# Optimization experiments

Hardware: AMD Instinct MI355X
Metric: run time of the kernel (lower is better)

The kernel has to match this reference:

```python
import math
import jax, jax.numpy as jnp
import numpy as np

SQ = 2048   # sequence length (hard-coded in source views)
B = 1       # batch (input_[:, 0, :] in QKVLinear)
H = 2048    # HIDDEN_SIZE
NH = 16     # NUM_HEADS
HD = 128    # head dim


def setup_inputs() -> dict:
    key = jax.random.key(0)
    ks = jax.random.split(key, 8)
    hidden_states = jax.random.normal(ks[0], (SQ, B, H), dtype=jnp.float32)
    # causal mask: True = masked (upper triangle, strictly above diagonal)
    attention_mask = jnp.triu(jnp.ones((SQ, SQ), dtype=bool), k=1)[None, None]
    qkv_w = jax.random.normal(ks[1], (3 * H, H), dtype=jnp.float32) * 0.02
    qkv_b = jax.random.normal(ks[2], (3 * H,), dtype=jnp.float32) * 0.02
    # SVD rotation matrices (approximately norm-preserving random matrices)
    svd_token = jax.random.normal(ks[3], (H, H), dtype=jnp.float32) / math.sqrt(H)
    svd_qk = jax.random.normal(ks[4], (NH, HD, HD), dtype=jnp.float32) / math.sqrt(HD)
    svd_vlin = jax.random.normal(ks[5], (NH, HD, HD), dtype=jnp.float32) / math.sqrt(HD)
    dense_w = jax.random.normal(ks[6], (NH, HD, H), dtype=jnp.float32) * 0.02
    dense_b = jax.random.normal(ks[7], (H,), dtype=jnp.float32) * 0.02
    return {
        "hidden_states": hidden_states,
        "attention_mask": attention_mask,
        "qkv_w": qkv_w,
        "qkv_b": qkv_b,
        "svd_token": svd_token,
        "svd_qk": svd_qk,
        "svd_vlin": svd_vlin,
        "dense_w": dense_w,
        "dense_b": dense_b,
    }


def reference(hidden_states, attention_mask, qkv_w, qkv_b, svd_token,
              svd_qk, svd_vlin, dense_w, dense_b):
    # QKVLinear: project input and weight through token-SVD (drop fraction = 0 -> no zeroing)
    x = hidden_states[:, 0, :] @ svd_token                 # [sq, H]
    w = qkv_w @ svd_token                                  # [3H, H]
    mixed = x @ w.T + qkv_b                                # [sq, 3H]
    mixed = mixed.reshape(SQ, B, NH, 3 * HD)
    q, k, v = jnp.split(mixed, 3, axis=-1)                 # each [sq, b, nh, hd]

    # per-head SVD-rotated Q/K (qk_drop = 0 -> h_mask is all-False, no zeroing)
    q = jnp.einsum('sbhd,hde->sbhe', q, svd_qk)
    k = jnp.einsum('sbhd,hde->sbhe', k, svd_qk)

    # scores: baddbmm with alpha = 1/(sqrt(hd)*coeff), then softmax rescales by coeff;
    # with layer_num=1 coeff=1, masked positions end at exactly -10000.
    scale = 1.0 / math.sqrt(HD)
    scores = jnp.einsum('sbhd,tbhd->bhst', q, k) * scale   # [b, nh, sq, sq]
    scores = jnp.where(attention_mask, -10000.0, scores)
    probs = jax.nn.softmax(scores, axis=-1)                # dropout in eval mode (identity)

    # per-head SVD-rotated V (vlinear_drop = 0 -> no zeroing)
    vv = jnp.einsum('sbhd,hde->sbhe', v, svd_vlin)
    ctx = jnp.einsum('bhst,tbhe->sbhe', probs, vv).reshape(SQ, B, H)

    # AttnOutputLinear: tsr block for head h = (dense_w[h].T @ svd_vlin[h]).T = svd_vlin[h].T @ dense_w[h]
    tsr = jnp.einsum('hde,hdo->heo', svd_vlin, dense_w).reshape(H, H)
    out = ctx @ tsr + dense_b                              # [sq, b, H]
    return out
```

## Files before the change

### kernel.cpp

```cpp
#include <hip/hip_runtime.h>
#include <hip/hip_bf16.h>
#include <stdint.h>
#include <math.h>


typedef __bf16 bf16_t;
typedef __bf16 bf16x8 __attribute__((ext_vector_type(8)));
typedef __bf16 bf16x4 __attribute__((ext_vector_type(4)));
typedef float  f32x4  __attribute__((ext_vector_type(4)));

__device__ __forceinline__ void async16(const void* g, void* l) {
  __builtin_amdgcn_global_load_lds(
      (const __attribute__((address_space(1))) void*)(uintptr_t)g,
      (__attribute__((address_space(3))) void*)(uint32_t)(uintptr_t)l,
      16, 0, 0);
}

__global__ __launch_bounds__(256)
void gemm_nt128(const bf16_t* __restrict__ A, const bf16_t* __restrict__ B,
                void* __restrict__ Cv, const void* __restrict__ biasv,
                int K, int lda, int ldb, int ldc, float alpha, int flags)
{
  const int bm0 = blockIdx.y * 128;
  const int bn0 = blockIdx.x * 128;

  __shared__ bf16_t shA[8192];
  __shared__ bf16_t shB[8192];

  const int t  = threadIdx.x;
  const int w  = t >> 6;
  const int l  = t & 63;
  const int wm = (w >> 1) * 64;
  const int wn = (w & 1) * 64;
  const int r0 = l >> 2;
  const int c0 = ((l & 3) ^ ((l >> 3) & 3)) * 8;
  const int fr = l & 15;
  const int kc = l >> 4;
  const int swr = ((fr >> 1) & 3);

  f32x4 acc[4][4];
  #pragma unroll
  for (int i = 0; i < 4; ++i)
    #pragma unroll
    for (int j = 0; j < 4; ++j)
      #pragma unroll
      for (int r = 0; r < 4; ++r)
        acc[i][j][r] = 0.0f;

  for (int k0 = 0; k0 < K; k0 += 64) {
    #pragma unroll
    for (int u = 0; u < 4; ++u) {
      const int seg  = u * 4 + w;
      const int half = seg >> 3;
      const int s8   = seg & 7;
      const int row  = s8 * 16 + r0;
      const int gk   = k0 + half * 32 + c0;
      async16(A + (long long)(bm0 + row) * lda + gk, &shA[half * 4096 + s8 * 512]);
      async16(B + (long long)(bn0 + row) * ldb + gk, &shB[half * 4096 + s8 * 512]);
    }
    __builtin_amdgcn_s_waitcnt(0);
    __syncthreads();

    const int rc = (kc ^ swr) * 8;
    #pragma unroll
    for (int h = 0; h < 2; ++h) {
      bf16x8 af[4], bfv[4];
      #pragma unroll
      for (int i = 0; i < 4; ++i) {
        af[i]  = *(const bf16x8*)&shA[h * 4096 + (wm + i * 16 + fr) * 32 + rc];
        bfv[i] = *(const bf16x8*)&shB[h * 4096 + (wn + i * 16 + fr) * 32 + rc];
      }
      #pragma unroll
      for (int i = 0; i < 4; ++i)
        #pragma unroll
        for (int j = 0; j < 4; ++j)
          acc[i][j] = __builtin_amdgcn_mfma_f32_16x16x32_bf16(af[i], bfv[j], acc[i][j], 0, 0, 0);
    }
    __syncthreads();
  }

  const int cc = l & 15;
  const int rq = (l >> 4) * 4;
  if (flags & 4) {
    float* C = (float*)Cv;
    const float* bias = (const float*)biasv;
    #pragma unroll
    for (int j = 0; j < 4; ++j) {
      const int col = bn0 + wn + j * 16 + cc;
      const float bv = bias ? bias[col] : 0.0f;
      #pragma unroll
      for (int i = 0; i < 4; ++i)
        #pragma unroll
        for (int r = 0; r < 4; ++r) {
          const int row = bm0 + wm + i * 16 + rq + r;
          C[(long long)row * ldc + col] = acc[i][j][r] * alpha + bv;
        }
    }
  } else {
    bf16_t* C = (bf16_t*)Cv;
    const bf16_t* bias = (flags & 8) ? (const bf16_t*)biasv : nullptr;
    #pragma unroll
    for (int j = 0; j < 4; ++j) {
      const int col = bn0 + wn + j * 16 + cc;
      const float bv = bias ? (float)bias[col] : 0.0f;
      #pragma unroll
      for (int i = 0; i < 4; ++i)
        #pragma unroll
        for (int r = 0; r < 4; ++r) {
          const int row = bm0 + wm + i * 16 + rq + r;
          C[(long long)row * ldc + col] = (bf16_t)(acc[i][j][r] * alpha + bv);
        }
    }
  }
}

__global__ __launch_bounds__(256)
void gemm_nt64(const bf16_t* __restrict__ A, const bf16_t* __restrict__ B,
               void* __restrict__ Cv, const void* __restrict__ biasv,
               int K, int lda, int ldb, int ldc, float alpha, int flags)
{
  const int bm0 = blockIdx.y * 64;
  const int bn0 = blockIdx.x * 128;

  __shared__ bf16_t shA[4096];
  __shared__ bf16_t shB[8192];

  const int t  = threadIdx.x;
  const int w  = t >> 6;
  const int l  = t & 63;
  const int wm = (w >> 1) * 32;
  const int wn = (w & 1) * 64;
  const int r0 = l >> 2;
  const int c0 = ((l & 3) ^ ((l >> 3) & 3)) * 8;
  const int fr = l & 15;
  const int kc = l >> 4;
  const int swr = ((fr >> 1) & 3);

  f32x4 acc[2][4];
  #pragma unroll
  for (int i = 0; i < 2; ++i)
    #pragma unroll
    for (int j = 0; j < 4; ++j)
      #pragma unroll
      for (int r = 0; r < 4; ++r)
        acc[i][j][r] = 0.0f;

  for (int k0 = 0; k0 < K; k0 += 64) {
    #pragma unroll
    for (int u = 0; u < 2; ++u) {
      const int seg  = u * 4 + w;
      const int half = seg >> 2;
      const int s4   = seg & 3;
      const int row  = s4 * 16 + r0;
      async16(A + (long long)(bm0 + row) * lda + (k0 + half * 32 + c0),
              &shA[half * 2048 + s4 * 512]);
    }
    #pragma unroll
    for (int u = 0; u < 4; ++u) {
      const int seg  = u * 4 + w;
      const int half = seg >> 3;
      const int s8   = seg & 7;
      const int row  = s8 * 16 + r0;
      async16(B + (long long)(bn0 + row) * ldb + (k0 + half * 32 + c0),
              &shB[half * 4096 + s8 * 512]);
    }
    __builtin_amdgcn_s_waitcnt(0);
    __syncthreads();

    const int rc = (kc ^ swr) * 8;
    #pragma unroll
    for (int h = 0; h < 2; ++h) {
      bf16x8 af[2], bfv[4];
      #pragma unroll
      for (int i = 0; i < 2; ++i)
        af[i]  = *(const bf16x8*)&shA[h * 2048 + (wm + i * 16 + fr) * 32 + rc];
      #pragma unroll
      for (int j = 0; j < 4; ++j)
        bfv[j] = *(const bf16x8*)&shB[h * 4096 + (wn + j * 16 + fr) * 32 + rc];
      #pragma unroll
      for (int i = 0; i < 2; ++i)
        #pragma unroll
        for (int j = 0; j < 4; ++j)
          acc[i][j] = __builtin_amdgcn_mfma_f32_16x16x32_bf16(af[i], bfv[j], acc[i][j], 0, 0, 0);
    }
    __syncthreads();
  }

  const int cc = l & 15;
  const int rq = (l >> 4) * 4;
  if (flags & 4) {
    float* C = (float*)Cv;
    const float* bias = (const float*)biasv;
    #pragma unroll
    for (int j = 0; j < 4; ++j) {
      const int col = bn0 + wn + j * 16 + cc;
      const float bv = bias ? bias[col] : 0.0f;
      #pragma unroll
      for (int i = 0; i < 2; ++i)
        #pragma unroll
        for (int r = 0; r < 4; ++r) {
          const int row = bm0 + wm + i * 16 + rq + r;
          C[(long long)row * ldc + col] = acc[i][j][r] * alpha + bv;
        }
    }
  } else {
    bf16_t* C = (bf16_t*)Cv;
    #pragma unroll
    for (int j = 0; j < 4; ++j) {
      const int col = bn0 + wn + j * 16 + cc;
      #pragma unroll
      for (int i = 0; i < 2; ++i)
        #pragma unroll
        for (int r = 0; r < 4; ++r) {
          const int row = bm0 + wm + i * 16 + rq + r;
          C[(long long)row * ldc + col] = (bf16_t)(acc[i][j][r] * alpha);
        }
    }
  }
}

__global__ __launch_bounds__(256)
void gemm_prep(const bf16_t* __restrict__ qkT, const bf16_t* __restrict__ vlT,
               const bf16_t* __restrict__ qkv_wT, const bf16_t* __restrict__ dwT,
               bf16_t* __restrict__ Wrot, bf16_t* __restrict__ tsrT)
{
  const int z = blockIdx.z;
  const bf16_t* A;
  const bf16_t* B;
  bf16_t* C;
  int bm0, bn0;
  if (z < 48) {
    const int h = z / 3, p = z - 3 * h;
    A = (p == 2 ? vlT : qkT) + h * 16384;
    B = qkv_wT + (long long)z * 262144;
    C = Wrot + (long long)z * 262144;
    bm0 = 0;
    bn0 = blockIdx.x * 128;
  } else {
    const int b = z - 48;
    A = dwT + (long long)b * 262144;
    B = vlT + b * 16384;
    C = tsrT;
    bm0 = blockIdx.x * 128;
    bn0 = b * 128;
  }

  __shared__ bf16_t shA[8192];
  __shared__ bf16_t shB[8192];

  const int t  = threadIdx.x;
  const int w  = t >> 6;
  const int l  = t & 63;
  const int wm = (w >> 1) * 64;
  const int wn = (w & 1) * 64;
  const int r0 = l >> 2;
  const int c0 = ((l & 3) ^ ((l >> 3) & 3)) * 8;
  const int fr = l & 15;
  const int kc = l >> 4;
  const int swr = ((fr >> 1) & 3);
  const int arow0 = (z < 48 ? 0 : bm0);
  const int brow0 = (z < 48 ? bn0 : 0);

  f32x4 acc[4][4];
  #pragma unroll
  for (int i = 0; i < 4; ++i)
    #pragma unroll
    for (int j = 0; j < 4; ++j)
      #pragma unroll
      for (int r = 0; r < 4; ++r)
        acc[i][j][r] = 0.0f;

  for (int k0 = 0; k0 < 128; k0 += 64) {
    #pragma unroll
    for (int u = 0; u < 4; ++u) {
      const int seg  = u * 4 + w;
      const int half = seg >> 3;
      const int s8   = seg & 7;
      const int row  = s8 * 16 + r0;
      const int gk   = k0 + half * 32 + c0;
      async16(A + (long long)(arow0 + row) * 128 + gk, &shA[half * 4096 + s8 * 512]);
      async16(B + (long long)(brow0 + row) * 128 + gk, &shB[half * 4096 + s8 * 512]);
    }
    __builtin_amdgcn_s_waitcnt(0);
    __syncthreads();

    const int rc = (kc ^ swr) * 8;
    #pragma unroll
    for (int h = 0; h < 2; ++h) {
      bf16x8 af[4], bfv[4];
      #pragma unroll
      for (int i = 0; i < 4; ++i) {
        af[i]  = *(const bf16x8*)&shA[h * 4096 + (wm + i * 16 + fr) * 32 + rc];
        bfv[i] = *(const bf16x8*)&shB[h * 4096 + (wn + i * 16 + fr) * 32 + rc];
      }
      #pragma unroll
      for (int i = 0; i < 4; ++i)
        #pragma unroll
        for (int j = 0; j < 4; ++j)
          acc[i][j] = __builtin_amdgcn_mfma_f32_16x16x32_bf16(af[i], bfv[j], acc[i][j], 0, 0, 0);
    }
    __syncthreads();
  }

  const int cc = l & 15;
  const int rq = (l >> 4) * 4;
  #pragma unroll
  for (int j = 0; j < 4; ++j) {
    const int col = bn0 + wn + j * 16 + cc;
    #pragma unroll
    for (int i = 0; i < 4; ++i)
      #pragma unroll
      for (int r = 0; r < 4; ++r) {
        const int row = arow0 + wm + i * 16 + rq + r;
        C[(long long)row * 2048 + col] = (bf16_t)acc[i][j][r];
      }
  }
}

__global__ __launch_bounds__(256)
void flash_k(const bf16_t* __restrict__ mixed, const bf16_t* __restrict__ vT,
             bf16_t* __restrict__ ctx, float iscale)
{
  const int h  = blockIdx.y;
  const int qt = 31 - (int)blockIdx.x;
  const int r0g = qt * 64;
  const int niter = (qt >> 1) + 1;
  const bf16_t* Qp = mixed + h * 384;
  const bf16_t* Kp = mixed + h * 384 + 128;
  const bf16_t* Vp = vT + (long long)h * 262144;

  __shared__ bf16_t sKV[128 * 128];
  __shared__ bf16_t sP[64 * 136];
  __shared__ float  sL[2][64];

  const int t  = threadIdx.x;
  const int w  = t >> 6;
  const int l  = t & 63;
  const int wm = (w >> 1) * 32;
  const int wn = (w & 1) * 64;
  const int fr = l & 15;
  const int kc = l >> 4;

  bf16x8 aq[2][4];
  #pragma unroll
  for (int i = 0; i < 2; ++i)
    #pragma unroll
    for (int ks = 0; ks < 4; ++ks)
      aq[i][ks] = *(const bf16x8*)(Qp + (long long)(r0g + wm + i * 16 + fr) * 6144
                                      + ks * 32 + kc * 8);

  f32x4 oacc[2][4];
  #pragma unroll
  for (int i = 0; i < 2; ++i)
    #pragma unroll
    for (int j = 0; j < 4; ++j)
      #pragma unroll
      for (int r = 0; r < 4; ++r) oacc[i][j][r] = 0.0f;
  float lsum[2][4];
  #pragma unroll
  for (int i = 0; i < 2; ++i)
    #pragma unroll
    for (int r = 0; r < 4; ++r) lsum[i][r] = 0.0f;

  for (int it = 0; it < niter; ++it) {
    const int t0 = it * 128;
    #pragma unroll
    for (int s = 0; s < 8; ++s) {
      const int chunk = (w * 8 + s) * 64 + l;
      const int r = chunk >> 4;
      const int c = (chunk & 15) ^ (r & 7);
      async16(Kp + (long long)(t0 + r) * 6144 + c * 8, &sKV[(w * 8 + s) * 512]);
    }
    __builtin_amdgcn_s_waitcnt(0);
    __syncthreads();

    f32x4 acc[2][4];
    #pragma unroll
    for (int i = 0; i < 2; ++i)
      #pragma unroll
      for (int j = 0; j < 4; ++j)
        #pragma unroll
        for (int r = 0; r < 4; ++r) acc[i][j][r] = 0.0f;
    #pragma unroll
    for (int ks = 0; ks < 4; ++ks) {
      bf16x8 bk[4];
      #pragma unroll
      for (int j = 0; j < 4; ++j) {
        const int r = wn + j * 16 + fr;
        const int c = (ks * 4 + kc) ^ (r & 7);
        bk[j] = *(const bf16x8*)&sKV[r * 128 + c * 8];
      }
      #pragma unroll
      for (int i = 0; i < 2; ++i)
        #pragma unroll
        for (int j = 0; j < 4; ++j)
          acc[i][j] = __builtin_amdgcn_mfma_f32_16x16x32_bf16(aq[i][ks], bk[j], acc[i][j], 0, 0, 0);
    }

    #pragma unroll
    for (int i = 0; i < 2; ++i) {
      #pragma unroll
      for (int r = 0; r < 4; ++r) {
        const int rowl = wm + i * 16 + kc * 4 + r;
        const int Rg = r0g + rowl;
        float rs = 0.f;
        #pragma unroll
        for (int j = 0; j < 4; ++j) {
          const int coll = wn + j * 16 + fr;
          const float e = (t0 + coll <= Rg) ? __expf(acc[i][j][r] * iscale) : 0.0f;
          rs += e;
          sP[rowl * 136 + coll] = (bf16_t)e;
        }
        rs += __shfl_xor(rs, 1, 64);
        rs += __shfl_xor(rs, 2, 64);
        rs += __shfl_xor(rs, 4, 64);
        rs += __shfl_xor(rs, 8, 64);
        if (fr == 0) sL[w & 1][rowl] = rs;
      }
    }
    __syncthreads();

    #pragma unroll
    for (int i = 0; i < 2; ++i)
      #pragma unroll
      for (int r = 0; r < 4; ++r) {
        const int rowl = wm + i * 16 + kc * 4 + r;
        lsum[i][r] += sL[0][rowl] + sL[1][rowl];
      }
    #pragma unroll
    for (int s = 0; s < 8; ++s) {
      const int chunk = (w * 8 + s) * 64 + l;
      const int r = chunk >> 4;
      const int c = (chunk & 15) ^ (r & 7);
      async16(Vp + (long long)r * 2048 + t0 + c * 8, &sKV[(w * 8 + s) * 512]);
    }
    __builtin_amdgcn_s_waitcnt(0);
    __syncthreads();

    #pragma unroll
    for (int ks = 0; ks < 4; ++ks) {
      bf16x8 ap[2], bv[4];
      #pragma unroll
      for (int i = 0; i < 2; ++i)
        ap[i] = *(const bf16x8*)&sP[(wm + i * 16 + fr) * 136 + ks * 32 + kc * 8];
      #pragma unroll
      for (int j = 0; j < 4; ++j) {
        const int r = wn + j * 16 + fr;
        const int c = (ks * 4 + kc) ^ (r & 7);
        bv[j] = *(const bf16x8*)&sKV[r * 128 + c * 8];
      }
      #pragma unroll
      for (int i = 0; i < 2; ++i)
        #pragma unroll
        for (int j = 0; j < 4; ++j)
          oacc[i][j] = __builtin_amdgcn_mfma_f32_16x16x32_bf16(ap[i], bv[j], oacc[i][j], 0, 0, 0);
    }
    __syncthreads();
  }

  #pragma unroll
  for (int i = 0; i < 2; ++i) {
    #pragma unroll
    for (int r = 0; r < 4; ++r) {
      const int rowl = wm + i * 16 + kc * 4 + r;
      const float inv = 1.0f / lsum[i][r];
      #pragma unroll
      for (int j = 0; j < 4; ++j) {
        const int coll = wn + j * 16 + fr;
        ctx[(long long)(r0g + rowl) * 2048 + h * 128 + coll] = (bf16_t)(oacc[i][j][r] * inv);
      }
    }
  }
}

__global__ __launch_bounds__(256)
void cvt2_f2b(const float* __restrict__ a, bf16_t* __restrict__ oa,
              const float* __restrict__ b, bf16_t* __restrict__ ob, int n)
{
  const float* in = blockIdx.y ? b : a;
  bf16_t* out = blockIdx.y ? ob : oa;
  const int i = (blockIdx.x * 256 + threadIdx.x) * 4;
  if (i >= n) return;
  const f32x4 v = *(const f32x4*)(in + i);
  bf16x4 o;
  #pragma unroll
  for (int j = 0; j < 4; ++j) o[j] = (bf16_t)v[j];
  *(bf16x4*)(out + i) = o;
}

__global__ __launch_bounds__(256)
void transpose_k2(const float* __restrict__ in1, const float* __restrict__ in2,
                  bf16_t* __restrict__ o1, bf16_t* __restrict__ o2)
{
  __shared__ bf16_t sm[32][33];
  const int z  = blockIdx.z;
  const float* ip = (z < 48) ? in1 + (long long)z * 262144
                             : in2 + (long long)(z - 48) * 262144;
  bf16_t* op = (z < 48) ? o1 + (long long)z * 262144
                        : o2 + (long long)(z - 48) * 262144;
  const int r0 = blockIdx.x << 5;
  const int c0 = blockIdx.y << 5;
  const int tx = threadIdx.x & 31;
  const int ty = threadIdx.x >> 5;
  #pragma unroll
  for (int yy = ty; yy < 32; yy += 8)
    sm[yy][tx] = (bf16_t)ip[(long long)(r0 + yy) * 2048 + c0 + tx];
  __syncthreads();
  #pragma unroll
  for (int yy = ty; yy < 32; yy += 8)
    op[(long long)(c0 + yy) * 128 + r0 + tx] = sm[tx][yy];
}

__global__ __launch_bounds__(256)
void transpose_rot(const float* __restrict__ qk, const float* __restrict__ vl,
                   bf16_t* __restrict__ oqk, bf16_t* __restrict__ ovl)
{
  __shared__ bf16_t sm[32][33];
  const int z  = blockIdx.z;
  const float* ip = (z < 16 ? qk : vl) + (long long)(z & 15) * 16384;
  bf16_t* op = (z < 16 ? oqk : ovl) + (long long)(z & 15) * 16384;
  const int r0 = blockIdx.x << 5;
  const int c0 = blockIdx.y << 5;
  const int tx = threadIdx.x & 31;
  const int ty = threadIdx.x >> 5;
  #pragma unroll
  for (int yy = ty; yy < 32; yy += 8)
    sm[yy][tx] = (bf16_t)ip[(long long)(r0 + yy) * 128 + c0 + tx];
  __syncthreads();
  #pragma unroll
  for (int yy = ty; yy < 32; yy += 8)
    op[(long long)(c0 + yy) * 128 + r0 + tx] = sm[tx][yy];
}

__global__ __launch_bounds__(256)
void transpose_b2b(const bf16_t* __restrict__ in, bf16_t* __restrict__ out,
                   int R, long long zsi, int rsi, long long zso)
{
  __shared__ bf16_t sm[32][33];
  const int z  = blockIdx.z;
  const int r0 = blockIdx.x << 5;
  const int c0 = blockIdx.y << 5;
  const int tx = threadIdx.x & 31;
  const int ty = threadIdx.x >> 5;
  const bf16_t* ip = in + (long long)z * zsi;
  bf16_t* op = out + (long long)z * zso;
  #pragma unroll
  for (int yy = ty; yy < 32; yy += 8)
    sm[yy][tx] = ip[(long long)(r0 + yy) * rsi + c0 + tx];
  __syncthreads();
  #pragma unroll
  for (int yy = ty; yy < 32; yy += 8)
    op[(long long)(c0 + yy) * R + r0 + tx] = sm[tx][yy];
}

__global__ void brot_k(const float* __restrict__ qkv_b,
                       const float* __restrict__ svd_qk,
                       const float* __restrict__ svd_vl,
                       bf16_t* __restrict__ brot)
{
  const int hp = blockIdx.x;
  const int h = hp / 3, p = hp % 3;
  const int e = threadIdx.x;
  const float* R = (p == 2 ? svd_vl : svd_qk) + h * 16384;
  const float* b = qkv_b + h * 384 + p * 128;
  float acc = 0.f;
  for (int d = 0; d < 128; ++d)
    acc += b[d] * R[d * 128 + e];
  brot[h * 384 + p * 128 + e] = (bf16_t)acc;
}

extern "C" void kernel_launch(void* const* d_in, const int* in_sizes, int n_in,
                              void* d_out, int out_size, void* d_ws, size_t ws_size,
                              hipStream_t stream)
{
  const float* hs      = (const float*)d_in[0];
  const float* qkv_w   = (const float*)d_in[2];
  const float* qkv_b   = (const float*)d_in[3];
  const float* svd_tok = (const float*)d_in[4];
  const float* svd_qk  = (const float*)d_in[5];
  const float* svd_vl  = (const float*)d_in[6];
  const float* dense_w = (const float*)d_in[7];
  const float* dense_b = (const float*)d_in[8];
  float* out = (float*)d_out;
  bf16_t* ws = (bf16_t*)d_ws;

  bf16_t* hsb    = ws;
  bf16_t* stb    = ws +  4194304LL;
  bf16_t* Mbuf   = ws +  8388608LL;
  bf16_t* x2     = ws + 12582912LL;
  bf16_t* qkv_wT = ws + 16777216LL;
  bf16_t* Wrot   = ws + 29360128LL;
  bf16_t* mixed  = ws + 41943040LL;
  bf16_t* vT     = ws + 54525952LL;
  bf16_t* ctx    = ws + 58720256LL;
  bf16_t* dwT    = ws + 62914560LL;
  bf16_t* tsrT   = ws + 67108864LL;
  bf16_t* qkT    = ws + 71303168LL;
  bf16_t* vlT    = ws + 71565312LL;
  bf16_t* brot   = ws + 71827456LL;
  if (ws_size < 71833600ULL * 2ULL) return;

  const float iscale = 0.08838834764831845f;

  cvt2_f2b<<<dim3(4096, 2), 256, 0, stream>>>(hs, hsb, svd_tok, stb, 4194304);
  transpose_rot<<<dim3(4, 4, 32), 256, 0, stream>>>(svd_qk, svd_vl, qkT, vlT);
  transpose_k2<<<dim3(4, 64, 64), 256, 0, stream>>>(qkv_w, dense_w, qkv_wT, dwT);
  brot_k<<<dim3(48), 128, 0, stream>>>(qkv_b, svd_qk, svd_vl, brot);

  gemm_nt64<<<dim3(16, 32), 256, 0, stream>>>(stb, stb, Mbuf, nullptr,
      2048, 2048, 2048, 2048, 1.0f, 0);
  gemm_nt64<<<dim3(16, 32), 256, 0, stream>>>(hsb, Mbuf, x2, nullptr,
      2048, 2048, 2048, 2048, 1.0f, 0);
  gemm_prep<<<dim3(16, 1, 64), 256, 0, stream>>>(qkT, vlT, qkv_wT, dwT, Wrot, tsrT);
  gemm_nt128<<<dim3(48, 16), 256, 0, stream>>>(x2, Wrot, mixed, brot,
      2048, 2048, 2048, 6144, 1.0f, 8);
  transpose_b2b<<<dim3(64, 4, 16), 256, 0, stream>>>(mixed + 256, vT, 2048, 384, 6144, 262144);
  flash_k<<<dim3(32, 16), 256, 0, stream>>>(mixed, vT, ctx, iscale);
  gemm_nt64<<<dim3(16, 32), 256, 0, stream>>>(ctx, tsrT, out, dense_b,
      2048, 2048, 2048, 2048, 1.0f, 4);
}
```

Before: 438.1 us.

## Merge prep kernels into fused launches and deepen GEMM K-tile

Folds the four preprocessing kernels (convert, two transposes, bias rotation) into one front kernel, and merges the weight-rotation GEMM with the svd_token Gram GEMM (stb·stbᵀ) into a single launch of 1536 blocks. The 64x128 GEMM now stages 128-wide K tiles per iteration instead of 64, halving its barrier count but doubling shared memory. The goal is fewer launches and better overlap of small independent work, at the cost of lower occupancy and a weight-transpose path that loops over 64 tiles per block with less parallelism.

```diff
diff --git a/kernel.cpp b/kernel.cpp
--- a/kernel.cpp
+++ b/kernel.cpp
@@ -81,49 +81,32 @@
 
   const int cc = l & 15;
   const int rq = (l >> 4) * 4;
-  if (flags & 4) {
-    float* C = (float*)Cv;
-    const float* bias = (const float*)biasv;
-    #pragma unroll
-    for (int j = 0; j < 4; ++j) {
-      const int col = bn0 + wn + j * 16 + cc;
-      const float bv = bias ? bias[col] : 0.0f;
-      #pragma unroll
-      for (int i = 0; i < 4; ++i)
-        #pragma unroll
-        for (int r = 0; r < 4; ++r) {
-          const int row = bm0 + wm + i * 16 + rq + r;
-          C[(long long)row * ldc + col] = acc[i][j][r] * alpha + bv;
-        }
-    }
-  } else {
-    bf16_t* C = (bf16_t*)Cv;
-    const bf16_t* bias = (flags & 8) ? (const bf16_t*)biasv : nullptr;
-    #pragma unroll
-    for (int j = 0; j < 4; ++j) {
-      const int col = bn0 + wn + j * 16 + cc;
-      const float bv = bias ? (float)bias[col] : 0.0f;
-      #pragma unroll
-      for (int i = 0; i < 4; ++i)
-        #pragma unroll
-        for (int r = 0; r < 4; ++r) {
-          const int row = bm0 + wm + i * 16 + rq + r;
-          C[(long long)row * ldc + col] = (bf16_t)(acc[i][j][r] * alpha + bv);
-        }
-    }
+  bf16_t* C = (bf16_t*)Cv;
+  const bf16_t* bias = (flags & 8) ? (const bf16_t*)biasv : nullptr;
+  #pragma unroll
+  for (int j = 0; j < 4; ++j) {
+    const int col = bn0 + wn + j * 16 + cc;
+    const float bv = bias ? (float)bias[col] : 0.0f;
+    #pragma unroll
+    for (int i = 0; i < 4; ++i)
+      #pragma unroll
+      for (int r = 0; r < 4; ++r) {
+        const int row = bm0 + wm + i * 16 + rq + r;
+        C[(long long)row * ldc + col] = (bf16_t)(acc[i][j][r] * alpha + bv);
+      }
   }
 }
 
 __global__ __launch_bounds__(256)
-void gemm_nt64(const bf16_t* __restrict__ A, const bf16_t* __restrict__ B,
-               void* __restrict__ Cv, const void* __restrict__ biasv,
-               int K, int lda, int ldb, int ldc, float alpha, int flags)
+void gemm_nt64k(const bf16_t* __restrict__ A, const bf16_t* __restrict__ B,
+                void* __restrict__ Cv, const void* __restrict__ biasv,
+                int K, int lda, int ldb, int ldc, float alpha, int flags)
 {
   const int bm0 = blockIdx.y * 64;
   const int bn0 = blockIdx.x * 128;
 
-  __shared__ bf16_t shA[4096];
-  __shared__ bf16_t shB[8192];
+  __shared__ bf16_t shA[8192];
+  __shared__ bf16_t shB[16384];
 
   const int t  = threadIdx.x;
   const int w  = t >> 6;
@@ -145,38 +128,36 @@
       for (int r = 0; r < 4; ++r)
         acc[i][j][r] = 0.0f;
 
-  for (int k0 = 0; k0 < K; k0 += 64) {
-    #pragma unroll
-    for (int u = 0; u < 2; ++u) {
-      const int seg  = u * 4 + w;
-      const int half = seg >> 2;
-      const int s4   = seg & 3;
-      const int row  = s4 * 16 + r0;
-      async16(A + (long long)(bm0 + row) * lda + (k0 + half * 32 + c0),
-              &shA[half * 2048 + s4 * 512]);
-    }
+  for (int k0 = 0; k0 < K; k0 += 128) {
     #pragma unroll
     for (int u = 0; u < 4; ++u) {
-      const int seg  = u * 4 + w;
-      const int half = seg >> 3;
-      const int s8   = seg & 7;
-      const int row  = s8 * 16 + r0;
-      async16(B + (long long)(bn0 + row) * ldb + (k0 + half * 32 + c0),
-              &shB[half * 4096 + s8 * 512]);
+      const int seg = u * 4 + w;
+      const int q   = seg >> 2;
+      const int s4  = seg & 3;
+      async16(A + (long long)(bm0 + s4 * 16 + r0) * lda + (k0 + q * 32 + c0),
+              &shA[q * 2048 + s4 * 512]);
+    }
+    #pragma unroll
+    for (int u = 0; u < 8; ++u) {
+      const int seg = u * 4 + w;
+      const int q   = seg >> 3;
+      const int s8  = seg & 7;
+      async16(B + (long long)(bn0 + s8 * 16 + r0) * ldb + (k0 + q * 32 + c0),
+              &shB[q * 4096 + s8 * 512]);
     }
     __builtin_amdgcn_s_waitcnt(0);
     __syncthreads();
 
     const int rc = (kc ^ swr) * 8;
     #pragma unroll
-    for (int h = 0; h < 2; ++h) {
+    for (int q = 0; q < 4; ++q) {
       bf16x8 af[2], bfv[4];
       #pragma unroll
       for (int i = 0; i < 2; ++i)
-        af[i]  = *(const bf16x8*)&shA[h * 2048 + (wm + i * 16 + fr) * 32 + rc];
+        af[i]  = *(const bf16x8*)&shA[q * 2048 + (wm + i * 16 + fr) * 32 + rc];
       #pragma unroll
       for (int j = 0; j < 4; ++j)
-        bfv[j] = *(const bf16x8*)&shB[h * 4096 + (wn + j * 16 + fr) * 32 + rc];
+        bfv[j] = *(const bf16x8*)&shB[q * 4096 + (wn + j * 16 + fr) * 32 + rc];
       #pragma unroll
       for (int i = 0; i < 2; ++i)
         #pragma unroll
@@ -220,100 +201,170 @@
 }
 
 __global__ __launch_bounds__(256)
-void gemm_prep(const bf16_t* __restrict__ qkT, const bf16_t* __restrict__ vlT,
-               const bf16_t* __restrict__ qkv_wT, const bf16_t* __restrict__ dwT,
-               bf16_t* __restrict__ Wrot, bf16_t* __restrict__ tsrT)
+void gemm_mprep(const bf16_t* __restrict__ qkT, const bf16_t* __restrict__ vlT,
+                const bf16_t* __restrict__ qkv_wT, const bf16_t* __restrict__ dwT,
+                bf16_t* __restrict__ Wrot, bf16_t* __restrict__ tsrT,
+                const bf16_t* __restrict__ stb, bf16_t* __restrict__ Mbuf)
 {
-  const int z = blockIdx.z;
-  const bf16_t* A;
-  const bf16_t* B;
-  bf16_t* C;
-  int bm0, bn0;
-  if (z < 48) {
-    const int h = z / 3, p = z - 3 * h;
-    A = (p == 2 ? vlT : qkT) + h * 16384;
-    B = qkv_wT + (long long)z * 262144;
-    C = Wrot + (long long)z * 262144;
-    bm0 = 0;
-    bn0 = blockIdx.x * 128;
-  } else {
-    const int b = z - 48;
-    A = dwT + (long long)b * 262144;
-    B = vlT + b * 16384;
-    C = tsrT;
-    bm0 = blockIdx.x * 128;
-    bn0 = b * 128;
-  }
-
-  __shared__ bf16_t shA[8192];
-  __shared__ bf16_t shB[8192];
-
+  __shared__ bf16_t smem[16384];
+  const int z = blockIdx.x;
   const int t  = threadIdx.x;
   const int w  = t >> 6;
   const int l  = t & 63;
-  const int wm = (w >> 1) * 64;
-  const int wn = (w & 1) * 64;
   const int r0 = l >> 2;
   const int c0 = ((l & 3) ^ ((l >> 3) & 3)) * 8;
   const int fr = l & 15;
   const int kc = l >> 4;
   const int swr = ((fr >> 1) & 3);
-  const int arow0 = (z < 48 ? 0 : bm0);
-  const int brow0 = (z < 48 ? bn0 : 0);
-
-  f32x4 acc[4][4];
-  #pragma unroll
-  for (int i = 0; i < 4; ++i)
-    #pragma unroll
-    for (int j = 0; j < 4; ++j)
-      #pragma unroll
-      for (int r = 0; r < 4; ++r)
-        acc[i][j][r] = 0.0f;
-
-  for (int k0 = 0; k0 < 128; k0 += 64) {
-    #pragma unroll
-    for (int u = 0; u < 4; ++u) {
-      const int seg  = u * 4 + w;
-      const int half = seg >> 3;
-      const int s8   = seg & 7;
-      const int row  = s8 * 16 + r0;
-      const int gk   = k0 + half * 32 + c0;
-      async16(A + (long long)(arow0 + row) * 128 + gk, &shA[half * 4096 + s8 * 512]);
-      async16(B + (long long)(brow0 + row) * 128 + gk, &shB[half * 4096 + s8 * 512]);
-    }
-    __builtin_amdgcn_s_waitcnt(0);
-    __syncthreads();
-
-    const int rc = (kc ^ swr) * 8;
-    #pragma unroll
-    for (int h = 0; h < 2; ++h) {
-      bf16x8 af[4], bfv[4];
-      #pragma unroll
-      for (int i = 0; i < 4; ++i) {
-        af[i]  = *(const bf16x8*)&shA[h * 4096 + (wm + i * 16 + fr) * 32 + rc];
-        bfv[i] = *(const bf16x8*)&shB[h * 4096 + (wn + i * 16 + fr) * 32 + rc];
-      }
-      #pragma unroll
-      for (int i = 0; i < 4; ++i)
-        #pragma unroll
-        for (int j = 0; j < 4; ++j)
-          acc[i][j] = __builtin_amdgcn_mfma_f32_16x16x32_bf16(af[i], bfv[j], acc[i][j], 0, 0, 0);
-    }
-    __syncthreads();
-  }
-
   const int cc = l & 15;
   const int rq = (l >> 4) * 4;
-  #pragma unroll
-  for (int j = 0; j < 4; ++j) {
-    const int col = bn0 + wn + j * 16 + cc;
+
+  if (z < 1024) {
+    const int pz = z >> 4, px = z & 15;
+    const bf16_t* A;
+    const bf16_t* B;
+    bf16_t* C;
+    int bm0, bn0;
+    if (pz < 48) {
+      const int h = pz / 3, p = pz - 3 * h;
+      A = (p == 2 ? vlT : qkT) + h * 16384;
+      B = qkv_wT + (long long)pz * 262144;
+      C = Wrot + (long long)pz * 262144;
+      bm0 = 0;  bn0 = px * 128;
+    } else {
+      const int b = pz - 48;
+      A = dwT + (long long)b * 262144;
+      B = vlT + b * 16384;
+      C = tsrT;
+      bm0 = px * 128;  bn0 = b * 128;
+    }
+    bf16_t* shA = smem;
+    bf16_t* shB = smem + 8192;
+    const int wm = (w >> 1) * 64;
+    const int wn = (w & 1) * 64;
+    const int arow0 = (pz < 48 ? 0 : bm0);
+    const int brow0 = (pz < 48 ? bn0 : 0);
+
+    f32x4 acc[4][4];
     #pragma unroll
     for (int i = 0; i < 4; ++i)
       #pragma unroll
-      for (int r = 0; r < 4; ++r) {
-        const int row = arow0 + wm + i * 16 + rq + r;
-        C[(long long)row * 2048 + col] = (bf16_t)acc[i][j][r];
-      }
+      for (int j = 0; j < 4; ++j)
+        #pragma unroll
+        for (int r = 0; r < 4; ++r)
+          acc[i][j][r] = 0.0f;
+
+    for (int k0 = 0; k0 < 128; k0 += 64) {
+      #pragma unroll
+      for (int u = 0; u < 4; ++u) {
+        const int seg  = u * 4 + w;
+        const int half = seg >> 3;
+        const int s8   = seg & 7;
+        const int row  = s8 * 16 + r0;
+        const int gk   = k0 + half * 32 + c0;
+        async16(A + (long long)(arow0 + row) * 128 + gk, &shA[half * 4096 + s8 * 512]);
+        async16(B + (long long)(brow0 + row) * 128 + gk, &shB[half * 4096 + s8 * 512]);
+      }
+      __builtin_amdgcn_s_waitcnt(0);
+      __syncthreads();
+
+      const int rc = (kc ^ swr) * 8;
+      #pragma unroll
+      for (int h = 0; h < 2; ++h) {
+        bf16x8 af[4], bfv[4];
+        #pragma unroll
+        for (int i = 0; i < 4; ++i) {
+          af[i]  = *(const bf16x8*)&shA[h * 4096 + (wm + i * 16 + fr) * 32 + rc];
+          bfv[i] = *(const bf16x8*)&shB[h * 4096 + (wn + i * 16 + fr) * 32 + rc];
+        }
+        #pragma unroll
+        for (int i = 0; i < 4; ++i)
+          #pragma unroll
+          for (int j = 0; j < 4; ++j)
+            acc[i][j] = __builtin_amdgcn_mfma_f32_16x16x32_bf16(af[i], bfv[j], acc[i][j], 0, 0, 0);
+      }
+      __syncthreads();
+    }
+
+    #pragma unroll
+    for (int j = 0; j < 4; ++j) {
+      const int col = bn0 + wn + j * 16 + cc;
+      #pragma unroll
+      for (int i = 0; i < 4; ++i)
+        #pragma unroll
+        for (int r = 0; r < 4; ++r) {
+          const int row = arow0 + wm + i * 16 + rq + r;
+          C[(long long)row * 2048 + col] = (bf16_t)acc[i][j][r];
+        }
+    }
+  } else {
+    const int m = z - 1024;
+    const int bm0 = (m >> 4) * 64;
+    const int bn0 = (m & 15) * 128;
+    bf16_t* shA = smem;
+    bf16_t* shB = smem + 4096;
+    const int wm = (w >> 1) * 32;
+    const int wn = (w & 1) * 64;
+
+    f32x4 acc[2][4];
+    #pragma unroll
+    for (int i = 0; i < 2; ++i)
+      #pragma unroll
+      for (int j = 0; j < 4; ++j)
+        #pragma unroll
+        for (int r = 0; r < 4; ++r)
+          acc[i][j][r] = 0.0f;
+
+    for (int k0 = 0; k0 < 2048; k0 += 64) {
+      #pragma unroll
+      for (int u = 0; u < 2; ++u) {
+        const int seg  = u * 4 + w;
+        const int half = seg >> 2;
+        const int s4   = seg & 3;
+        async16(stb + (long long)(bm0 + s4 * 16 + r0) * 2048 + (k0 + half * 32 + c0),
+                &shA[half * 2048 + s4 * 512]);
+      }
+      #pragma unroll
+      for (int u = 0; u < 4; ++u) {
+        const int seg  = u * 4 + w;
+        const int half = seg >> 3;
+        const int s8   = seg & 7;
+        async16(stb + (long long)(bn0 + s8 * 16 + r0) * 2048 + (k0 + half * 32 + c0),
+                &shB[half * 4096 + s8 * 512]);
+      }
+      __builtin_amdgcn_s_waitcnt(0);
+      __syncthreads();
+
+      const int rc = (kc ^ swr) * 8;
+      #pragma unroll
+      for (int h = 0; h < 2; ++h) {
+        bf16x8 af[2], bfv[4];
+        #pragma unroll
+        for (int i = 0; i < 2; ++i)
+          af[i]  = *(const bf16x8*)&shA[h * 2048 + (wm + i * 16 + fr) * 32 + rc];
+        #pragma unroll
+        for (int j = 0; j < 4; ++j)
+          bfv[j] = *(const bf16x8*)&shB[h * 4096 + (wn + j * 16 + fr) * 32 + rc];
+        #pragma unroll
+        for (int i = 0; i < 2; ++i)
+          #pragma unroll
+          for (int j = 0; j < 4; ++j)
+            acc[i][j] = __builtin_amdgcn_mfma_f32_16x16x32_bf16(af[i], bfv[j], acc[i][j], 0, 0, 0);
+      }
+      __syncthreads();
+    }
+
+    #pragma unroll
+    for (int j = 0; j < 4; ++j) {
+      const int col = bn0 + wn + j * 16 + cc;
+      #pragma unroll
+      for (int i = 0; i < 2; ++i)
+        #pragma unroll
+        for (int r = 0; r < 4; ++r) {
+          const int row = bm0 + wm + i * 16 + rq + r;
+          Mbuf[(long long)row * 2048 + col] = (bf16_t)acc[i][j][r];
+        }
+    }
   }
 }
 
@@ -474,62 +525,80 @@
 }
 
 __global__ __launch_bounds__(256)
-void cvt2_f2b(const float* __restrict__ a, bf16_t* __restrict__ oa,
-              const float* __restrict__ b, bf16_t* __restrict__ ob, int n)
-{
-  const float* in = blockIdx.y ? b : a;
-  bf16_t* out = blockIdx.y ? ob : oa;
-  const int i = (blockIdx.x * 256 + threadIdx.x) * 4;
-  if (i >= n) return;
-  const f32x4 v = *(const f32x4*)(in + i);
-  bf16x4 o;
-  #pragma unroll
-  for (int j = 0; j < 4; ++j) o[j] = (bf16_t)v[j];
-  *(bf16x4*)(out + i) = o;
-}
-
-__global__ __launch_bounds__(256)
-void transpose_k2(const float* __restrict__ in1, const float* __restrict__ in2,
-                  bf16_t* __restrict__ o1, bf16_t* __restrict__ o2)
+void front_k(const float* __restrict__ hs, bf16_t* __restrict__ hsb,
+             const float* __restrict__ svd_tok, bf16_t* __restrict__ stb,
+             const float* __restrict__ svd_qk, bf16_t* __restrict__ qkT,
+             const float* __restrict__ svd_vl, bf16_t* __restrict__ vlT,
+             const float* __restrict__ qkv_w, bf16_t* __restrict__ qkv_wT,
+             const float* __restrict__ dense_w, bf16_t* __restrict__ dwT,
+             const float* __restrict__ qkv_b, bf16_t* __restrict__ brot)
 {
   __shared__ bf16_t sm[32][33];
-  const int z  = blockIdx.z;
-  const float* ip = (z < 48) ? in1 + (long long)z * 262144
-                             : in2 + (long long)(z - 48) * 262144;
-  bf16_t* op = (z < 48) ? o1 + (long long)z * 262144
-                        : o2 + (long long)(z - 48) * 262144;
-  const int r0 = blockIdx.x << 5;
-  const int c0 = blockIdx.y << 5;
-  const int tx = threadIdx.x & 31;
-  const int ty = threadIdx.x >> 5;
-  #pragma unroll
-  for (int yy = ty; yy < 32; yy += 8)
-    sm[yy][tx] = (bf16_t)ip[(long long)(r0 + yy) * 2048 + c0 + tx];
-  __syncthreads();
-  #pragma unroll
-  for (int yy = ty; yy < 32; yy += 8)
-    op[(long long)(c0 + yy) * 128 + r0 + tx] = sm[tx][yy];
-}
-
-__global__ __launch_bounds__(256)
-void transpose_rot(const float* __restrict__ qk, const float* __restrict__ vl,
-                   bf16_t* __restrict__ oqk, bf16_t* __restrict__ ovl)
-{
-  __shared__ bf16_t sm[32][33];
-  const int z  = blockIdx.z;
-  const float* ip = (z < 16 ? qk : vl) + (long long)(z & 15) * 16384;
-  bf16_t* op = (z < 16 ? oqk : ovl) + (long long)(z & 15) * 16384;
-  const int r0 = blockIdx.x << 5;
-  const int c0 = blockIdx.y << 5;
-  const int tx = threadIdx.x & 31;
-  const int ty = threadIdx.x >> 5;
-  #pragma unroll
-  for (int yy = ty; yy < 32; yy += 8)
-    sm[yy][tx] = (bf16_t)ip[(long long)(r0 + yy) * 128 + c0 + tx];
-  __syncthreads();
-  #pragma unroll
-  for (int yy = ty; yy < 32; yy += 8)
-    op[(long long)(c0 + yy) * 128 + r0 + tx] = sm[tx][yy];
+  const int z = blockIdx.x;
+  const int tid = threadIdx.x;
+
+  if (z < 2048) {
+    const float* in = (z < 1024) ? hs : svd_tok;
+    bf16_t* out = (z < 1024) ? hsb : stb;
+    const int base = (z & 1023) * 4096 + tid * 16;
+    #pragma unroll
+    for (int j = 0; j < 4; ++j) {
+      const f32x4 v = *(const f32x4*)(in + base + j * 4);
+      bf16x4 o;
+      #pragma unroll
+      for (int k = 0; k < 4; ++k) o[k] = (bf16_t)v[k];
+      *(bf16x4*)(out + base + j * 4) = o;
+    }
+  } else if (z < 2560) {
+    const int zz = z - 2048;
+    const int zr = zz >> 4;
+    const int tile = zz & 15;
+    const float* ip = (zr < 16 ? svd_qk : svd_vl) + (long long)(zr & 15) * 16384;
+    bf16_t* op = (zr < 16 ? qkT : vlT) + (long long)(zr & 15) * 16384;
+    const int r0 = (tile & 3) << 5;
+    const int c0 = (tile >> 2) << 5;
+    const int tx = tid & 31;
+    const int ty = tid >> 5;
+    #pragma unroll
+    for (int yy = ty; yy < 32; yy += 8)
+      sm[yy][tx] = (bf16_t)ip[(long long)(r0 + yy) * 128 + c0 + tx];
+    __syncthreads();
+    #pragma unroll
+    for (int yy = ty; yy < 32; yy += 8)
+      op[(long long)(c0 + yy) * 128 + r0 + tx] = sm[tx][yy];
+  } else if (z < 2816) {
+    const int zz = z - 2560;
+    const int zb = zz >> 2;
+    const int rt = zz & 3;
+    const float* ip = (zb < 48) ? qkv_w + (long long)zb * 262144
+                                : dense_w + (long long)(zb - 48) * 262144;
+    bf16_t* op = (zb < 48) ? qkv_wT + (long long)zb * 262144
+                           : dwT + (long long)(zb - 48) * 262144;
+    const int r0 = rt << 5;
+    const int tx = tid & 31;
+    const int ty = tid >> 5;
+    for (int ct = 0; ct < 64; ++ct) {
+      const int c0 = ct << 5;
+      #pragma unroll
+      for (int yy = ty; yy < 32; yy += 8)
+        sm[yy][tx] = (bf16_t)ip[(long long)(r0 + yy) * 2048 + c0 + tx];
+      __syncthreads();
+      #pragma unroll
+      for (int yy = ty; yy < 32; yy += 8)
+        op[(long long)(c0 + yy) * 128 + r0 + tx] = sm[tx][yy];
+      __syncthreads();
+    }
+  } else {
+    const int hp = (z - 2816) * 2 + (tid >> 7);
+    const int h = hp / 3, p = hp % 3;
+    const int e = tid & 127;
+    const float* R = (p == 2 ? (const float*)svd_vl : (const float*)svd_qk) + (long long)h * 16384;
+    const float* b = qkv_b + h * 384 + p * 128;
+    float acc = 0.f;
+    for (int d = 0; d < 128; ++d)
+      acc += b[d] * R[d * 128 + e];
+    brot[h * 384 + p * 128 + e] = (bf16_t)acc;
+  }
 }
 
 __global__ __launch_bounds__(256)
@@ -551,22 +620,6 @@
   #pragma unroll
   for (int yy = ty; yy < 32; yy += 8)
     op[(long long)(c0 + yy) * R + r0 + tx] = sm[tx][yy];
-}
-
-__global__ void brot_k(const float* __restrict__ qkv_b,
-                       const float* __restrict__ svd_qk,
-                       const float* __restrict__ svd_vl,
-                       bf16_t* __restrict__ brot)
-{
-  const int hp = blockIdx.x;
-  const int h = hp / 3, p = hp % 3;
-  const int e = threadIdx.x;
-  const float* R = (p == 2 ? svd_vl : svd_qk) + h * 16384;
-  const float* b = qkv_b + h * 384 + p * 128;
-  float acc = 0.f;
-  for (int d = 0; d < 128; ++d)
-    acc += b[d] * R[d * 128 + e];
-  brot[h * 384 + p * 128 + e] = (bf16_t)acc;
 }
 
 extern "C" void kernel_launch(void* const* d_in, const int* in_sizes, int n_in,
@@ -602,20 +655,16 @@
 
   const float iscale = 0.08838834764831845f;
 
-  cvt2_f2b<<<dim3(4096, 2), 256, 0, stream>>>(hs, hsb, svd_tok, stb, 4194304);
-  transpose_rot<<<dim3(4, 4, 32), 256, 0, stream>>>(svd_qk, svd_vl, qkT, vlT);
-  transpose_k2<<<dim3(4, 64, 64), 256, 0, stream>>>(qkv_w, dense_w, qkv_wT, dwT);
-  brot_k<<<dim3(48), 128, 0, stream>>>(qkv_b, svd_qk, svd_vl, brot);
-
-  gemm_nt64<<<dim3(16, 32), 256, 0, stream>>>(stb, stb, Mbuf, nullptr,
+  front_k<<<dim3(2840), 256, 0, stream>>>(hs, hsb, svd_tok, stb,
+      svd_qk, qkT, svd_vl, vlT, qkv_w, qkv_wT, dense_w, dwT, qkv_b, brot);
+  gemm_mprep<<<dim3(1536), 256, 0, stream>>>(qkT, vlT, qkv_wT, dwT,
+      Wrot, tsrT, stb, Mbuf);
+  gemm_nt64k<<<dim3(16, 32), 256, 0, stream>>>(hsb, Mbuf, x2, nullptr,
       2048, 2048, 2048, 2048, 1.0f, 0);
-  gemm_nt64<<<dim3(16, 32), 256, 0, stream>>>(hsb, Mbuf, x2, nullptr,
-      2048, 2048, 2048, 2048, 1.0f, 0);
-  gemm_prep<<<dim3(16, 1, 64), 256, 0, stream>>>(qkT, vlT, qkv_wT, dwT, Wrot, tsrT);
   gemm_nt128<<<dim3(48, 16), 256, 0, stream>>>(x2, Wrot, mixed, brot,
       2048, 2048, 2048, 6144, 1.0f, 8);
   transpose_b2b<<<dim3(64, 4, 16), 256, 0, stream>>>(mixed + 256, vT, 2048, 384, 6144, 262144);
   flash_k<<<dim3(32, 16), 256, 0, stream>>>(mixed, vT, ctx, iscale);
-  gemm_nt64<<<dim3(16, 32), 256, 0, stream>>>(ctx, tsrT, out, dense_b,
+  gemm_nt64k<<<dim3(16, 32), 256, 0, stream>>>(ctx, tsrT, out, dense_b,
       2048, 2048, 2048, 2048, 1.0f, 4);
 }
```

Measured after the change: 511.9 us. 1.17x slower.
